# Kernel optimization log

Measured on AMD Instinct MI355X. Metric: run time of the kernel, lower is better.

## Reference

```python
import jax, jax.numpy as jnp
import numpy as np

B, C, H, W = 4, 256, 128, 128
HEADS = 64
HD = C // HEADS  # 4
G = 32           # group norm groups
EPS = 1e-5


def setup_inputs() -> dict:
    key = jax.random.key(0)
    ks = jax.random.split(key, 6)
    x = jax.random.normal(ks[0], (B, C, H, W), dtype=jnp.float32)
    gn_weight = jnp.ones((1, C, 1, 1), dtype=jnp.float32)
    gn_bias = jnp.zeros((1, C, 1, 1), dtype=jnp.float32)
    # 1x1 convs stored as (out_ch, in_ch) matrices
    qkv_w = jax.random.normal(ks[1], (3 * C, C), dtype=jnp.float32) * 0.02
    qkv_b = jax.random.normal(ks[2], (3 * C,), dtype=jnp.float32) * 0.01
    out_w = jax.random.normal(ks[3], (C, C), dtype=jnp.float32) * 0.02
    out_b = jax.random.normal(ks[4], (C,), dtype=jnp.float32) * 0.01
    return {"x": x, "gn_weight": gn_weight, "gn_bias": gn_bias,
            "qkv_w": qkv_w, "qkv_b": qkv_b, "out_w": out_w, "out_b": out_b}


def group_norm(x, weight, bias):
    n, c, h, w = x.shape
    xg = x.reshape(n, G, -1)
    mean = xg.mean(axis=-1, keepdims=True)
    var = jnp.var(xg, axis=-1, keepdims=True, ddof=1)  # torch.var default is unbiased
    xg = (xg - mean) / jnp.sqrt(var + EPS)
    return xg.reshape(n, c, h, w) * weight + bias


def conv1x1(x, w, b):
    # x: (B, Cin, H, W), w: (Cout, Cin)
    return jnp.einsum('bchw,oc->bohw', x, w) + b[None, :, None, None]


def reference(x, gn_weight, gn_bias, qkv_w, qkv_b, out_w, out_b):
    skip = x
    h = group_norm(x, gn_weight, gn_bias)
    qkv = conv1x1(h, qkv_w, qkv_b)                      # (B, 3C, H, W)
    qkv = qkv.reshape(B, HEADS, 3 * HD, H * W)
    q, k, v = jnp.split(qkv, 3, axis=2)                  # each (B, heads, hd, HW)
    scores = jnp.einsum('bhdn,bhen->bhde', q, k) / (HD ** 0.5)  # (B, heads, hd, hd)
    scores = jax.nn.softmax(scores, axis=1)              # softmax over HEADS axis (as in source)
    out = jnp.einsum('bhde,bhen->bhdn', scores, v)       # (B, heads, hd, HW)
    out = out.reshape(B, C, H, W)
    out = conv1x1(out, out_w, out_b)
    return out + skip
```

## Files before the change

kernel.cpp:

```cpp
#include <hip/hip_runtime.h>


constexpr int kB = 4;
constexpr int kC = 256;
constexpr int kHW = 16384;
constexpr int kHeads = 64;
constexpr int kNG = 32;
constexpr int kCPG = 8;
constexpr int kCP1 = 257;
constexpr int kPS = 260;
constexpr float kEPS = 1e-5f;
constexpr int kNSplit = 32;

typedef __attribute__((ext_vector_type(8))) _Float16 f16x8;
typedef __attribute__((ext_vector_type(4))) _Float16 f16x4;
typedef __attribute__((ext_vector_type(4))) float f32x4;

union V8 { f16x8 v; uint4 u; _Float16 h[8]; };

__device__ __forceinline__ void gload16(const void* g, void* l) {
  __builtin_amdgcn_global_load_lds(
      (const __attribute__((address_space(1))) void*)g,
      (__attribute__((address_space(3))) void*)l, 16, 0, 0);
}

constexpr size_t oXT    = 0;
constexpr size_t oXH    = oXT + (size_t)kB * kHW * kC / 2;
constexpr size_t oSpart = oXH + (size_t)kB * kHW * kC / 2;
constexpr size_t oS     = oSpart + (size_t)3 * kB * kNSplit * 128 * 128;
constexpr size_t oSums  = oS + (size_t)kB * kCP1 * kPS;
constexpr size_t oGv    = oSums + (size_t)kB * kC;
constexpr size_t oScore = oGv + (size_t)kB * kC;
constexpr size_t oM     = oXH;
constexpr size_t oGmH   = oXH + (size_t)kB * kC * kPS;

__global__ __launch_bounds__(256) void k0_tr(const float* __restrict__ x,
                                             _Float16* __restrict__ xT,
                                             _Float16* __restrict__ xH,
                                             float* __restrict__ sums) {
  const int nt = blockIdx.x, ct = blockIdx.y, b = blockIdx.z;
  __shared__ float T[64][65];
  const float* xb = x + ((size_t)b * kC + ct * 64) * kHW + nt * 64;
  _Float16* xhb = xH + ((size_t)b * kC + ct * 64) * kHW + nt * 64;
  const int tid = threadIdx.x;
  const int lane = tid & 63;

#pragma unroll
  for (int rep = 0; rep < 2; ++rep) {
    const int r = rep * 32 + (tid >> 3);
    const int c8 = (tid & 7) * 8;
    float4 v0 = *(const float4*)(xb + (size_t)r * kHW + c8);
    float4 v1 = *(const float4*)(xb + (size_t)r * kHW + c8 + 4);
    T[r][c8 + 0] = v0.x; T[r][c8 + 1] = v0.y; T[r][c8 + 2] = v0.z; T[r][c8 + 3] = v0.w;
    T[r][c8 + 4] = v1.x; T[r][c8 + 5] = v1.y; T[r][c8 + 6] = v1.z; T[r][c8 + 7] = v1.w;
    V8 h;
    h.h[0] = (_Float16)v0.x; h.h[1] = (_Float16)v0.y;
    h.h[2] = (_Float16)v0.z; h.h[3] = (_Float16)v0.w;
    h.h[4] = (_Float16)v1.x; h.h[5] = (_Float16)v1.y;
    h.h[6] = (_Float16)v1.z; h.h[7] = (_Float16)v1.w;
    *(uint4*)(xhb + (size_t)r * kHW + c8) = h.u;
    float rs = v0.x + v0.y + v0.z + v0.w + v1.x + v1.y + v1.z + v1.w;
    rs += __shfl_xor(rs, 1);
    rs += __shfl_xor(rs, 2);
    rs += __shfl_xor(rs, 4);
    if ((lane & 7) == 0) atomicAdd(&sums[b * kC + ct * 64 + r], rs);
  }
  __syncthreads();
  const int nl = tid >> 2, cgrp = tid & 3;
  V8 lo, hi;
#pragma unroll
  for (int i = 0; i < 8; ++i)  lo.h[i] = (_Float16)T[cgrp * 16 + i][nl];
#pragma unroll
  for (int i = 0; i < 8; ++i)  hi.h[i] = (_Float16)T[cgrp * 16 + 8 + i][nl];
  _Float16* dst = xT + ((size_t)b * kHW + nt * 64 + nl) * kC + ct * 64 + cgrp * 16;
  *(uint4*)dst = lo.u;
  *(uint4*)(dst + 8) = hi.u;
}

__global__ __launch_bounds__(256) void k1_syrk(const _Float16* __restrict__ xH,
                                               float* __restrict__ Spart) {
  const int tt = blockIdx.x >> 5;
  const int sp = blockIdx.x & 31;
  const int b = blockIdx.y;
  const int ti = (tt == 2) ? 1 : 0;
  const int tj = (tt == 0) ? 0 : 1;
  const bool diag = (ti == tj);
  const _Float16* xb = xH + (size_t)b * kC * kHW;
  const int n0 = sp * (kHW / kNSplit);

  __shared__ __align__(16) _Float16 XI[2][128 * 64];
  __shared__ __align__(16) _Float16 XJ[2][128 * 64];

  const int tid = threadIdx.x;
  const int wave = tid >> 6, lane = tid & 63;
  const int wi = wave >> 1, wj = wave & 1;
  const int lrow = lane & 15, lgq = lane >> 4;
  const int srow = lane >> 3, sslot = lane & 7;

  const _Float16* srcI = xb + (size_t)(ti * 128) * kHW + n0;
  const _Float16* srcJ = xb + (size_t)(tj * 128) * kHW + n0;

  f32x4 acc[16];
#pragma unroll
  for (int i = 0; i < 16; ++i) acc[i] = (f32x4){0.f, 0.f, 0.f, 0.f};

  auto stage = [&](int buf, int nb) {
#pragma unroll
    for (int rep = 0; rep < 4; ++rep) {
      const int rr = rep * 32 + wave * 8 + srow;
      const int g = sslot ^ (rr & 7);
      char* dI = (char*)XI[buf] + (rep * 32 + wave * 8) * 128;
      gload16(srcI + (size_t)rr * kHW + nb + g * 8, dI);
      if (!diag) {
        char* dJ = (char*)XJ[buf] + (rep * 32 + wave * 8) * 128;
        gload16(srcJ + (size_t)rr * kHW + nb + g * 8, dJ);
      }
    }
  };

  stage(0, 0);
  __syncthreads();

  constexpr int NCH = kHW / kNSplit / 64;
  for (int ch = 0; ch < NCH; ++ch) {
    const int buf = ch & 1;
    if (ch + 1 < NCH) stage(buf ^ 1, (ch + 1) * 64);
    const _Float16* XIb = XI[buf];
    const _Float16* XBb = diag ? XI[buf] : XJ[buf];
#pragma unroll
    for (int sub = 0; sub < 2; ++sub) {
      const int gq = sub * 4 + lgq;
      f16x8 afr[4], bfr[4];
#pragma unroll
      for (int ia = 0; ia < 4; ++ia) {
        const int r = wi * 64 + ia * 16 + lrow;
        afr[ia] = *(const f16x8*)((const char*)XIb + (size_t)r * 128 + (((unsigned)(gq ^ (r & 7))) << 4));
      }
#pragma unroll
      for (int jb = 0; jb < 4; ++jb) {
        const int r = wj * 64 + jb * 16 + lrow;
        bfr[jb] = *(const f16x8*)((const char*)XBb + (size_t)r * 128 + (((unsigned)(gq ^ (r & 7))) << 4));
      }
#pragma unroll
      for (int ia = 0; ia < 4; ++ia)
#pragma unroll
        for (int jb = 0; jb < 4; ++jb)
          acc[ia * 4 + jb] = __builtin_amdgcn_mfma_f32_16x16x32_f16(afr[ia], bfr[jb], acc[ia * 4 + jb], 0, 0, 0);
    }
    __syncthreads();
  }
  float* P = Spart + (((size_t)tt * kB + b) * kNSplit + sp) * 16384;
#pragma unroll
  for (int ia = 0; ia < 4; ++ia)
#pragma unroll
    for (int jb = 0; jb < 4; ++jb)
#pragma unroll
      for (int reg = 0; reg < 4; ++reg) {
        const int i = wi * 64 + ia * 16 + lgq * 4 + reg;
        const int j = wj * 64 + jb * 16 + lrow;
        P[(size_t)i * 128 + j] = acc[ia * 4 + jb][reg];
      }
}

__global__ __launch_bounds__(256) void k1r_reduce(const float* __restrict__ Spart,
                                                  float* __restrict__ S) {
  const int blk = blockIdx.x;
  const int tile12 = blk >> 5;
  const int part = blk & 31;
  const int tt = tile12 >> 2, b = tile12 & 3;
  const int rti = (tt == 2) ? 1 : 0;
  const int rtj = (tt == 0) ? 0 : 1;
  const int e0 = part * 512 + threadIdx.x * 2;
  float2 s = {0.f, 0.f};
  const float* base = Spart + ((size_t)tt * kB + b) * kNSplit * 16384 + e0;
#pragma unroll 8
  for (int sp = 0; sp < kNSplit; ++sp) {
    float2 v = *(const float2*)(base + (size_t)sp * 16384);
    s.x += v.x; s.y += v.y;
  }
  const int i = e0 >> 7, j = e0 & 127;
  float* Sb = S + (size_t)b * kCP1 * kPS;
  float* dst = Sb + (size_t)(rti * 128 + i) * kPS + rtj * 128 + j;
  dst[0] = s.x; dst[1] = s.y;
  if (tt == 1) {
    Sb[(size_t)(128 + j + 0) * kPS + i] = s.x;
    Sb[(size_t)(128 + j + 1) * kPS + i] = s.y;
  }
}

__global__ __launch_bounds__(256) void k3ab(const float* __restrict__ S,
                                            const float* __restrict__ sums,
                                            const float* __restrict__ gw,
                                            const float* __restrict__ gb,
                                            const float* __restrict__ qkv_w,
                                            const float* __restrict__ qkv_b,
                                            float* __restrict__ score) {
  const int h = blockIdx.x, b = blockIdx.y;
  const float* Sb = S + (size_t)b * kCP1 * kPS;
  const float HWf = (float)kHW;
  __shared__ float shx[kC], shd[kC];
  __shared__ float meanv[kNG], invv[kNG];
  __shared__ float4 suw[kC];
  __shared__ float redPQ[4][8];
  __shared__ float red16[4][16];
  const int tid = threadIdx.x;
  const int wave = tid >> 6, lane = tid & 63;

  shx[tid] = sums[b * kC + tid];
  shd[tid] = Sb[(size_t)tid * kPS + tid];
  __syncthreads();
  if (tid < kNG) {
    float sum = 0.f, ssq = 0.f;
#pragma unroll
    for (int k = 0; k < kCPG; ++k) { sum += shx[tid * kCPG + k]; ssq += shd[tid * kCPG + k]; }
    const float n = (float)(kCPG * kHW);
    const float mean = sum / n;
    const float var = (ssq - n * mean * mean) / (n - 1.0f);
    meanv[tid] = mean;
    invv[tid] = rsqrtf(var + kEPS);
  }
  __syncthreads();
  const float s_c = gw[tid] * invv[tid / kCPG];
  const float t_c = gb[tid] - meanv[tid / kCPG] * s_c;
  const float x_c = shx[tid];
  const float r_c = s_c * x_c + t_c * HWf;

  const float u0 = qkv_w[(size_t)(h * 12 + 0) * kC + tid];
  const float u1 = qkv_w[(size_t)(h * 12 + 1) * kC + tid];
  const float u2 = qkv_w[(size_t)(h * 12 + 2) * kC + tid];
  const float u3 = qkv_w[(size_t)(h * 12 + 3) * kC + tid];
  const float v0 = qkv_w[(size_t)(h * 12 + 4) * kC + tid];
  const float v1 = qkv_w[(size_t)(h * 12 + 5) * kC + tid];
  const float v2 = qkv_w[(size_t)(h * 12 + 6) * kC + tid];
  const float v3 = qkv_w[(size_t)(h * 12 + 7) * kC + tid];
  suw[tid] = make_float4(u0 * s_c, u1 * s_c, u2 * s_c, u3 * s_c);

  float p[8] = {u0 * s_c * x_c, u1 * s_c * x_c, u2 * s_c * x_c, u3 * s_c * x_c,
                u0 * t_c, u1 * t_c, u2 * t_c, u3 * t_c};
#pragma unroll
  for (int i = 0; i < 8; ++i)
#pragma unroll
    for (int off = 32; off; off >>= 1) p[i] += __shfl_xor(p[i], off);
  if (lane == 0) {
#pragma unroll
    for (int i = 0; i < 8; ++i) redPQ[wave][i] = p[i];
  }
  __syncthreads();
  float P[4], Qp[4];
#pragma unroll
  for (int d = 0; d < 4; ++d) {
    P[d]  = redPQ[0][d] + redPQ[1][d] + redPQ[2][d] + redPQ[3][d];
    Qp[d] = redPQ[0][4 + d] + redPQ[1][4 + d] + redPQ[2][4 + d] + redPQ[3][4 + d]
            + qkv_b[h * 12 + d];
  }

  float sd0 = 0.f, sd1 = 0.f, sd2 = 0.f, sd3 = 0.f;
#pragma unroll 8
  for (int c = 0; c < kC; ++c) {
    const float Sval = Sb[(size_t)c * kPS + tid];
    const float4 w = suw[c];
    sd0 += w.x * Sval; sd1 += w.y * Sval; sd2 += w.z * Sval; sd3 += w.w * Sval;
  }
  float wd[4];
#pragma unroll
  for (int d = 0; d < 4; ++d) {
    const float sdv = (d == 0) ? sd0 : (d == 1) ? sd1 : (d == 2) ? sd2 : sd3;
    wd[d] = s_c * sdv + t_c * P[d] + r_c * Qp[d];
  }
  const float sv[4] = {v0, v1, v2, v3};
  float pr[16];
#pragma unroll
  for (int d = 0; d < 4; ++d)
#pragma unroll
    for (int e = 0; e < 4; ++e) pr[d * 4 + e] = wd[d] * sv[e];
#pragma unroll
  for (int i = 0; i < 16; ++i)
#pragma unroll
    for (int off = 32; off; off >>= 1) pr[i] += __shfl_xor(pr[i], off);
  if (lane == 0) {
#pragma unroll
    for (int i = 0; i < 16; ++i) red16[wave][i] = pr[i];
  }
  __syncthreads();
  if (tid < 16) {
    const int d = tid >> 2, e = tid & 3;
    float tot = red16[0][tid] + red16[1][tid] + red16[2][tid] + red16[3][tid];
    const float w256 = P[d] + HWf * Qp[d];
    tot += w256 * qkv_b[h * 12 + 4 + e];
    score[((size_t)(b * kHeads) + h) * 16 + tid] = 0.5f * tot;
  }
}

__global__ __launch_bounds__(256) void k45_M(const float* __restrict__ score,
                                             const float* __restrict__ qkv_w,
                                             const float* __restrict__ qkv_b,
                                             float* __restrict__ M) {
  const int b = blockIdx.y;
  const int cidx = blockIdx.x;
  const int h = cidx >> 2, d = cidx & 3;
  __shared__ float sc[64][4];
  __shared__ float mx[4], sm[4];
  const int tid = threadIdx.x;
  {
    const int h2 = tid >> 2, e = tid & 3;
    sc[h2][e] = score[((size_t)(b * kHeads) + h2) * 16 + d * 4 + e];
  }
  __syncthreads();
  const int wave = tid >> 6, lane = tid & 63;
  {
    const float v = sc[lane][wave];
    float m = v;
#pragma unroll
    for (int off = 32; off; off >>= 1) m = fmaxf(m, __shfl_xor(m, off));
    float e2 = expf(v - m);
#pragma unroll
    for (int off = 32; off; off >>= 1) e2 += __shfl_xor(e2, off);
    if (lane == 0) { mx[wave] = m; sm[wave] = e2; }
  }
  __syncthreads();
  const float p0 = expf(sc[h][0] - mx[0]) / sm[0];
  const float p1 = expf(sc[h][1] - mx[1]) / sm[1];
  const float p2 = expf(sc[h][2] - mx[2]) / sm[2];
  const float p3 = expf(sc[h][3] - mx[3]) / sm[3];
  for (int cp = tid; cp < kCP1; cp += 256) {
    float a;
    if (cp < kC) {
      a = p0 * qkv_w[(size_t)(h * 12 + 8 + 0) * kC + cp] +
          p1 * qkv_w[(size_t)(h * 12 + 8 + 1) * kC + cp] +
          p2 * qkv_w[(size_t)(h * 12 + 8 + 2) * kC + cp] +
          p3 * qkv_w[(size_t)(h * 12 + 8 + 3) * kC + cp];
    } else {
      a = p0 * qkv_b[h * 12 + 8 + 0] + p1 * qkv_b[h * 12 + 8 + 1] +
          p2 * qkv_b[h * 12 + 8 + 2] + p3 * qkv_b[h * 12 + 8 + 3];
    }
    M[((size_t)b * kC + cidx) * kPS + cp] = a;
  }
}

__global__ __launch_bounds__(256) void k5b_gemm(const float* __restrict__ M,
                                                const float* __restrict__ out_w,
                                                const float* __restrict__ S,
                                                const float* __restrict__ sums,
                                                const float* __restrict__ gw,
                                                const float* __restrict__ gb,
                                                _Float16* __restrict__ GmH,
                                                float* __restrict__ gvec) {
  const int ct = blockIdx.x, ot = blockIdx.y, b = blockIdx.z;
  const float* Mb = M + (size_t)b * kC * kPS;
  const float* Sb = S + (size_t)b * kCP1 * kPS;
  __shared__ float Wt[32][68];
  __shared__ float Gs[32][68];
  __shared__ float gred[64][17];
  __shared__ float sS[kC], sT[kC];
  __shared__ float meanv[kNG], invv[kNG];
  const int tid = threadIdx.x;
  sS[tid] = sums[b * kC + tid];
  sT[tid] = Sb[(size_t)tid * kPS + tid];
  __syncthreads();
  if (tid < kNG) {
    float sum = 0.f, ssq = 0.f;
#pragma unroll
    for (int k = 0; k < kCPG; ++k) { sum += sS[tid * kCPG + k]; ssq += sT[tid * kCPG + k]; }
    const float n = (float)(kCPG * kHW);
    const float mean = sum / n;
    const float var = (ssq - n * mean * mean) / (n - 1.0f);
    meanv[tid] = mean;
    invv[tid] = rsqrtf(var + kEPS);
  }
  __syncthreads();
  {
    const float sv = gw[tid] * invv[tid / kCPG];
    sS[tid] = sv;
    sT[tid] = gb[tid] - meanv[tid / kCPG] * sv;
  }
  __syncthreads();
  float acc[16];
#pragma unroll
  for (int i = 0; i < 16; ++i) acc[i] = 0.f;
  const int i0 = (tid & 15) * 4;
  const int j0 = (tid >> 4) * 4;
  const int cp0 = ct * 64;

  for (int cb = 0; cb < kC; cb += 32) {
    int idx = tid;
#pragma unroll
    for (int r = 0; r < 2; ++r) {
      const int m = idx >> 3;
      const int c4 = (idx & 7) * 4;
      float4 v = *(const float4*)(out_w + (size_t)(ot * 64 + m) * kC + cb + c4);
      Wt[c4 + 0][m] = v.x; Wt[c4 + 1][m] = v.y; Wt[c4 + 2][m] = v.z; Wt[c4 + 3][m] = v.w;
      idx += 256;
    }
    idx = tid;
#pragma unroll
    for (int r = 0; r < 2; ++r) {
      const int cc = idx >> 4;
      const int n4 = (idx & 15) * 4;
      float4 v = {0.f, 0.f, 0.f, 0.f};
      if (cp0 + n4 < kCP1) v = *(const float4*)(Mb + (size_t)(cb + cc) * kPS + cp0 + n4);
      *(float4*)&Gs[cc][n4] = v;
      idx += 256;
    }
    __syncthreads();
#pragma unroll
    for (int kk = 0; kk < 32; ++kk) {
      float4 a = *(const float4*)&Wt[kk][i0];
      float4 g = *(const float4*)&Gs[kk][j0];
      acc[0]  += a.x * g.x; acc[1]  += a.x * g.y; acc[2]  += a.x * g.z; acc[3]  += a.x * g.w;
      acc[4]  += a.y * g.x; acc[5]  += a.y * g.y; acc[6]  += a.y * g.z; acc[7]  += a.y * g.w;
      acc[8]  += a.z * g.x; acc[9]  += a.z * g.y; acc[10] += a.z * g.z; acc[11] += a.z * g.w;
      acc[12] += a.w * g.x; acc[13] += a.w * g.y; acc[14] += a.w * g.z; acc[15] += a.w * g.w;
    }
    __syncthreads();
  }
  float gpart[4] = {0.f, 0.f, 0.f, 0.f};
#pragma unroll
  for (int mi = 0; mi < 4; ++mi) {
    const int o = ot * 64 + i0 + mi;
#pragma unroll
    for (int cj = 0; cj < 4; ++cj) {
      const int cp = cp0 + j0 + cj;
      const float f = acc[mi * 4 + cj];
      if (cp < kC) {
        GmH[((size_t)b * kC + o) * kC + cp] = (_Float16)(f * sS[cp]);
        gpart[mi] += f * sT[cp];
      } else if (cp == kC) {
        gpart[mi] += f;
      }
    }
  }
#pragma unroll
  for (int mi = 0; mi < 4; ++mi) gred[i0 + mi][tid >> 4] = gpart[mi];
  __syncthreads();
  if (tid < 64) {
    float s = 0.f;
#pragma unroll
    for (int k = 0; k < 16; ++k) s += gred[tid][k];
    atomicAdd(&gvec[b * kC + ot * 64 + tid], s);
  }
}

__global__ __launch_bounds__(256) void k6_final(const _Float16* __restrict__ xT,
                                                const _Float16* __restrict__ GmH,
                                                const float* __restrict__ gvec,
                                                const float* __restrict__ out_b,
                                                const float* __restrict__ x,
                                                float* __restrict__ out) {
  const int nt = blockIdx.x, ot = blockIdx.y, b = blockIdx.z;
  __shared__ __align__(16) char smem[64 * 132 * 4];
  _Float16* GT = (_Float16*)smem;
  _Float16* XT = (_Float16*)(smem + 16384);
  float* Ep = (float*)smem;
  const int tid = threadIdx.x;
  const int wave = tid >> 6, lane = tid & 63;
  const int wo = wave >> 1, wn = wave & 1;
  const int lrow = lane & 15, lgq = lane >> 4;

  f32x4 acc[16];
#pragma unroll
  for (int i = 0; i < 16; ++i) acc[i] = (f32x4){0.f, 0.f, 0.f, 0.f};

  for (int cc = 0; cc < kC; cc += 64) {
#pragma unroll
    for (int rep = 0; rep < 4; ++rep) {
      const int gi = tid + rep * 256;
      const int r = gi >> 3, g = gi & 7;
      const size_t boff = (size_t)r * 128 + (((unsigned)(g ^ (r & 7))) << 4);
      uint4 gv = *(const uint4*)(GmH + ((size_t)(b * kC + ot * 128 + r)) * kC + cc + g * 8);
      *(uint4*)((char*)GT + boff) = gv;
      uint4 xv = *(const uint4*)(xT + ((size_t)b * kHW + nt * 128 + r) * kC + cc + g * 8);
      *(uint4*)((char*)XT + boff) = xv;
    }
    __syncthreads();
#pragma unroll
    for (int sub = 0; sub < 2; ++sub) {
      const int gq = sub * 4 + lgq;
      f16x8 afr[4], bfr[4];
#pragma unroll
      for (int ia = 0; ia < 4; ++ia) {
        const int r = wo * 64 + ia * 16 + lrow;
        afr[ia] = *(const f16x8*)((const char*)GT + (size_t)r * 128 + (((unsigned)(gq ^ (r & 7))) << 4));
      }
#pragma unroll
      for (int jb = 0; jb < 4; ++jb) {
        const int r = wn * 64 + jb * 16 + lrow;
        bfr[jb] = *(const f16x8*)((const char*)XT + (size_t)r * 128 + (((unsigned)(gq ^ (r & 7))) << 4));
      }
#pragma unroll
      for (int ia = 0; ia < 4; ++ia)
#pragma unroll
        for (int jb = 0; jb < 4; ++jb)
          acc[ia * 4 + jb] = __builtin_amdgcn_mfma_f32_16x16x32_f16(afr[ia], bfr[jb], acc[ia * 4 + jb], 0, 0, 0);
    }
    __syncthreads();
  }
#pragma unroll
  for (int p = 0; p < 2; ++p) {
    if (wo == p) {
#pragma unroll
      for (int ia = 0; ia < 4; ++ia)
#pragma unroll
        for (int jb = 0; jb < 4; ++jb)
#pragma unroll
          for (int reg = 0; reg < 4; ++reg)
            Ep[(size_t)(ia * 16 + lgq * 4 + reg) * 132 + wn * 64 + jb * 16 + lrow] =
                acc[ia * 4 + jb][reg];
    }
    __syncthreads();
#pragma unroll
    for (int it = 0; it < 8; ++it) {
      const int id = it * 256 + tid;
      const int row = id >> 5, nc = (id & 31) * 4;
      const int o = ot * 128 + p * 64 + row;
      const float gvv = gvec[b * kC + o] + out_b[o];
      float4 e = *(const float4*)&Ep[(size_t)row * 132 + nc];
      const size_t gidx = ((size_t)b * kC + o) * kHW + nt * 128 + nc;
      float4 sk = *(const float4*)&x[gidx];
      float4 res = {e.x + gvv + sk.x, e.y + gvv + sk.y, e.z + gvv + sk.z, e.w + gvv + sk.w};
      *(float4*)&out[gidx] = res;
    }
    __syncthreads();
  }
}

extern "C" void kernel_launch(void* const* d_in, const int* in_sizes, int n_in,
                              void* d_out, int out_size, void* d_ws, size_t ws_size,
                              hipStream_t stream) {
  const float* x    = (const float*)d_in[0];
  const float* gnw  = (const float*)d_in[1];
  const float* gnb  = (const float*)d_in[2];
  const float* qkvw = (const float*)d_in[3];
  const float* qkvb = (const float*)d_in[4];
  const float* outw = (const float*)d_in[5];
  const float* outb = (const float*)d_in[6];
  float* out = (float*)d_out;
  float* ws = (float*)d_ws;

  _Float16* xT   = (_Float16*)(ws + oXT);
  _Float16* xH   = (_Float16*)(ws + oXH);
  float* Spart   = ws + oSpart;
  float* S       = ws + oS;
  float* sums    = ws + oSums;
  float* gv      = ws + oGv;
  float* score   = ws + oScore;
  float* M       = ws + oM;
  _Float16* GmH  = (_Float16*)(ws + oGmH);

  hipMemsetAsync(sums, 0, (size_t)2 * kB * kC * sizeof(float), stream);
  k0_tr<<<dim3(kHW / 64, kC / 64, kB), 256, 0, stream>>>(x, xT, xH, sums);
  k1_syrk<<<dim3(3 * kNSplit, kB), 256, 0, stream>>>(xH, Spart);
  k1r_reduce<<<dim3(3 * kB * 32), 256, 0, stream>>>(Spart, S);
  k3ab<<<dim3(kHeads, kB), 256, 0, stream>>>(S, sums, gnw, gnb, qkvw, qkvb, score);
  k45_M<<<dim3(kC, kB), 256, 0, stream>>>(score, qkvw, qkvb, M);
  k5b_gemm<<<dim3(5, 4, kB), 256, 0, stream>>>(M, outw, S, sums, gnw, gnb, GmH, gv);
  k6_final<<<dim3(kHW / 128, kC / 128, kB), 256, 0, stream>>>(xT, GmH, gv, outb, x, out);
}
```

Measured before the change: 230.7 us.

## Drop transposed fp16 copy of x; transpose channel-major tiles in final GEMM's LDS staging

The first kernel no longer writes a second, transposed fp16 copy of x. It only casts x to channel-major fp16 and accumulates per-channel sums with a block-level reduction, so each block issues one atomic per channel. The final GEMM now loads channel-major xH rows and scatters individual halves into its swizzled LDS tile, with a swizzle that also XORs r>>3. This saves one full fp16 write of x and its later read layout, at the cost of many 2-byte LDS stores (possible bank conflicts) in the final kernel. The M/GmH workspace is also moved off the xH region so it is no longer aliased.

```diff
diff --git a/kernel.cpp b/kernel.cpp
--- a/kernel.cpp
+++ b/kernel.cpp
@@ -24,57 +24,44 @@
       (__attribute__((address_space(3))) void*)l, 16, 0, 0);
 }
 
-constexpr size_t oXT    = 0;
-constexpr size_t oXH    = oXT + (size_t)kB * kHW * kC / 2;
+constexpr size_t oXH    = 0;
 constexpr size_t oSpart = oXH + (size_t)kB * kHW * kC / 2;
 constexpr size_t oS     = oSpart + (size_t)3 * kB * kNSplit * 128 * 128;
 constexpr size_t oSums  = oS + (size_t)kB * kCP1 * kPS;
 constexpr size_t oGv    = oSums + (size_t)kB * kC;
 constexpr size_t oScore = oGv + (size_t)kB * kC;
-constexpr size_t oM     = oXH;
-constexpr size_t oGmH   = oXH + (size_t)kB * kC * kPS;
-
-__global__ __launch_bounds__(256) void k0_tr(const float* __restrict__ x,
-                                             _Float16* __restrict__ xT,
-                                             _Float16* __restrict__ xH,
-                                             float* __restrict__ sums) {
-  const int nt = blockIdx.x, ct = blockIdx.y, b = blockIdx.z;
-  __shared__ float T[64][65];
-  const float* xb = x + ((size_t)b * kC + ct * 64) * kHW + nt * 64;
-  _Float16* xhb = xH + ((size_t)b * kC + ct * 64) * kHW + nt * 64;
+constexpr size_t oM     = oScore + (size_t)kB * kHeads * 16;
+constexpr size_t oGmH   = oM + (size_t)kB * kC * kPS;
+
+__global__ __launch_bounds__(256) void k0_cast(const float* __restrict__ x,
+                                               _Float16* __restrict__ xH,
+                                               float* __restrict__ sums) {
+  const int seg = blockIdx.x, c = blockIdx.y, b = blockIdx.z;
   const int tid = threadIdx.x;
-  const int lane = tid & 63;
-
-#pragma unroll
-  for (int rep = 0; rep < 2; ++rep) {
-    const int r = rep * 32 + (tid >> 3);
-    const int c8 = (tid & 7) * 8;
-    float4 v0 = *(const float4*)(xb + (size_t)r * kHW + c8);
-    float4 v1 = *(const float4*)(xb + (size_t)r * kHW + c8 + 4);
-    T[r][c8 + 0] = v0.x; T[r][c8 + 1] = v0.y; T[r][c8 + 2] = v0.z; T[r][c8 + 3] = v0.w;
-    T[r][c8 + 4] = v1.x; T[r][c8 + 5] = v1.y; T[r][c8 + 6] = v1.z; T[r][c8 + 7] = v1.w;
-    V8 h;
-    h.h[0] = (_Float16)v0.x; h.h[1] = (_Float16)v0.y;
-    h.h[2] = (_Float16)v0.z; h.h[3] = (_Float16)v0.w;
-    h.h[4] = (_Float16)v1.x; h.h[5] = (_Float16)v1.y;
-    h.h[6] = (_Float16)v1.z; h.h[7] = (_Float16)v1.w;
-    *(uint4*)(xhb + (size_t)r * kHW + c8) = h.u;
-    float rs = v0.x + v0.y + v0.z + v0.w + v1.x + v1.y + v1.z + v1.w;
-    rs += __shfl_xor(rs, 1);
-    rs += __shfl_xor(rs, 2);
-    rs += __shfl_xor(rs, 4);
-    if ((lane & 7) == 0) atomicAdd(&sums[b * kC + ct * 64 + r], rs);
-  }
-  __syncthreads();
-  const int nl = tid >> 2, cgrp = tid & 3;
-  V8 lo, hi;
-#pragma unroll
-  for (int i = 0; i < 8; ++i)  lo.h[i] = (_Float16)T[cgrp * 16 + i][nl];
-#pragma unroll
-  for (int i = 0; i < 8; ++i)  hi.h[i] = (_Float16)T[cgrp * 16 + 8 + i][nl];
-  _Float16* dst = xT + ((size_t)b * kHW + nt * 64 + nl) * kC + ct * 64 + cgrp * 16;
-  *(uint4*)dst = lo.u;
-  *(uint4*)(dst + 8) = hi.u;
+  const size_t base = ((size_t)b * kC + c) * kHW + (size_t)seg * 4096 + tid * 16;
+  float4 v0 = *(const float4*)(x + base);
+  float4 v1 = *(const float4*)(x + base + 4);
+  float4 v2 = *(const float4*)(x + base + 8);
+  float4 v3 = *(const float4*)(x + base + 12);
+  V8 h0, h1;
+  h0.h[0] = (_Float16)v0.x; h0.h[1] = (_Float16)v0.y;
+  h0.h[2] = (_Float16)v0.z; h0.h[3] = (_Float16)v0.w;
+  h0.h[4] = (_Float16)v1.x; h0.h[5] = (_Float16)v1.y;
+  h0.h[6] = (_Float16)v1.z; h0.h[7] = (_Float16)v1.w;
+  h1.h[0] = (_Float16)v2.x; h1.h[1] = (_Float16)v2.y;
+  h1.h[2] = (_Float16)v2.z; h1.h[3] = (_Float16)v2.w;
+  h1.h[4] = (_Float16)v3.x; h1.h[5] = (_Float16)v3.y;
+  h1.h[6] = (_Float16)v3.z; h1.h[7] = (_Float16)v3.w;
+  *(uint4*)(xH + base) = h0.u;
+  *(uint4*)(xH + base + 8) = h1.u;
+  float rs = (v0.x + v0.y + v0.z + v0.w) + (v1.x + v1.y + v1.z + v1.w) +
+             (v2.x + v2.y + v2.z + v2.w) + (v3.x + v3.y + v3.z + v3.w);
+#pragma unroll
+  for (int off = 32; off; off >>= 1) rs += __shfl_xor(rs, off);
+  __shared__ float ps[4];
+  if ((tid & 63) == 0) ps[tid >> 6] = rs;
+  __syncthreads();
+  if (tid == 0) atomicAdd(&sums[b * kC + c], ps[0] + ps[1] + ps[2] + ps[3]);
 }
 
 __global__ __launch_bounds__(256) void k1_syrk(const _Float16* __restrict__ xH,
@@ -440,7 +427,7 @@
   }
 }
 
-__global__ __launch_bounds__(256) void k6_final(const _Float16* __restrict__ xT,
+__global__ __launch_bounds__(256) void k6_final(const _Float16* __restrict__ xH,
                                                 const _Float16* __restrict__ GmH,
                                                 const float* __restrict__ gvec,
                                                 const float* __restrict__ out_b,
@@ -455,6 +442,7 @@
   const int wave = tid >> 6, lane = tid & 63;
   const int wo = wave >> 1, wn = wave & 1;
   const int lrow = lane & 15, lgq = lane >> 4;
+  const int xc = tid >> 2, xq = tid & 3;
 
   f32x4 acc[16];
 #pragma unroll
@@ -465,11 +453,24 @@
     for (int rep = 0; rep < 4; ++rep) {
       const int gi = tid + rep * 256;
       const int r = gi >> 3, g = gi & 7;
-      const size_t boff = (size_t)r * 128 + (((unsigned)(g ^ (r & 7))) << 4);
+      const size_t boff = (size_t)r * 128 + (((unsigned)(g ^ ((r ^ (r >> 3)) & 7))) << 4);
       uint4 gv = *(const uint4*)(GmH + ((size_t)(b * kC + ot * 128 + r)) * kC + cc + g * 8);
       *(uint4*)((char*)GT + boff) = gv;
-      uint4 xv = *(const uint4*)(xT + ((size_t)b * kHW + nt * 128 + r) * kC + cc + g * 8);
-      *(uint4*)((char*)XT + boff) = xv;
+    }
+    {
+      const _Float16* xrow = xH + ((size_t)b * kC + cc + xc) * kHW + nt * 128;
+#pragma unroll
+      for (int rep = 0; rep < 4; ++rep) {
+        const int n0 = rep * 32 + xq * 8;
+        V8 hx; hx.u = *(const uint4*)(xrow + n0);
+#pragma unroll
+        for (int k = 0; k < 8; ++k) {
+          const int n = n0 + k;
+          *(_Float16*)((char*)XT + (size_t)n * 128 +
+                       (((unsigned)((xc >> 3) ^ ((n ^ (n >> 3)) & 7))) << 4) +
+                       (xc & 7) * 2) = hx.h[k];
+        }
+      }
     }
     __syncthreads();
 #pragma unroll
@@ -479,12 +480,14 @@
 #pragma unroll
       for (int ia = 0; ia < 4; ++ia) {
         const int r = wo * 64 + ia * 16 + lrow;
-        afr[ia] = *(const f16x8*)((const char*)GT + (size_t)r * 128 + (((unsigned)(gq ^ (r & 7))) << 4));
+        afr[ia] = *(const f16x8*)((const char*)GT + (size_t)r * 128 +
+                                  (((unsigned)(gq ^ ((r ^ (r >> 3)) & 7))) << 4));
       }
 #pragma unroll
       for (int jb = 0; jb < 4; ++jb) {
         const int r = wn * 64 + jb * 16 + lrow;
-        bfr[jb] = *(const f16x8*)((const char*)XT + (size_t)r * 128 + (((unsigned)(gq ^ (r & 7))) << 4));
+        bfr[jb] = *(const f16x8*)((const char*)XT + (size_t)r * 128 +
+                                  (((unsigned)(gq ^ ((r ^ (r >> 3)) & 7))) << 4));
       }
 #pragma unroll
       for (int ia = 0; ia < 4; ++ia)
@@ -536,7 +539,6 @@
   float* out = (float*)d_out;
   float* ws = (float*)d_ws;
 
-  _Float16* xT   = (_Float16*)(ws + oXT);
   _Float16* xH   = (_Float16*)(ws + oXH);
   float* Spart   = ws + oSpart;
   float* S       = ws + oS;
@@ -547,11 +549,11 @@
   _Float16* GmH  = (_Float16*)(ws + oGmH);
 
   hipMemsetAsync(sums, 0, (size_t)2 * kB * kC * sizeof(float), stream);
-  k0_tr<<<dim3(kHW / 64, kC / 64, kB), 256, 0, stream>>>(x, xT, xH, sums);
+  k0_cast<<<dim3(4, kC, kB), 256, 0, stream>>>(x, xH, sums);
   k1_syrk<<<dim3(3 * kNSplit, kB), 256, 0, stream>>>(xH, Spart);
   k1r_reduce<<<dim3(3 * kB * 32), 256, 0, stream>>>(Spart, S);
   k3ab<<<dim3(kHeads, kB), 256, 0, stream>>>(S, sums, gnw, gnb, qkvw, qkvb, score);
   k45_M<<<dim3(kC, kB), 256, 0, stream>>>(score, qkvw, qkvb, M);
   k5b_gemm<<<dim3(5, 4, kB), 256, 0, stream>>>(M, outw, S, sums, gnw, gnb, GmH, gv);
-  k6_final<<<dim3(kHW / 128, kC / 128, kB), 256, 0, stream>>>(xT, GmH, gv, outb, x, out);
-}
+  k6_final<<<dim3(kHW / 128, kC / 128, kB), 256, 0, stream>>>(xH, GmH, gv, outb, x, out);
+}
```

Measured after the change: 208.5 us. 1.11x faster.
